# Kernel optimization log

Measured on AMD Instinct MI355X. Metric: run time of the kernel, lower is better.

Reference implementation:

```python
import jax, jax.numpy as jnp
import numpy as np

B, C, H, W = 16, 256, 96, 96
P = 16          # num_prototypes
G = 8           # GroupNorm groups
EPS = 1e-5


def setup_inputs() -> dict:
    key = jax.random.key(0)
    ks = jax.random.split(key, 18)
    n = jax.random.normal
    return {
        "x": n(ks[0], (B, C, H, W), jnp.float32),
        "prototypes": n(ks[1], (1, P, C), jnp.float32),
        "pos_embed": n(ks[2], (1, C, 64, 64), jnp.float32) * 0.02,
        "q_w": n(ks[3], (C, C), jnp.float32) * (C ** -0.5),
        "q_b": n(ks[4], (C,), jnp.float32) * 0.01,
        "k_w": n(ks[5], (C, C), jnp.float32) * (C ** -0.5),
        "k_b": n(ks[6], (C,), jnp.float32) * 0.01,
        "v_w": n(ks[7], (C, C), jnp.float32) * (C ** -0.5),
        "v_b": n(ks[8], (C,), jnp.float32) * 0.01,
        "out_w": n(ks[9], (C, C), jnp.float32) * (C ** -0.5),
        "out_b": n(ks[10], (C,), jnp.float32) * 0.01,
        "dw_w": n(ks[11], (C, 1, 3, 3), jnp.float32) * (1.0 / 3.0),  # depthwise 3x3, no bias
        "bn_g": 1.0 + 0.1 * n(ks[12], (C,), jnp.float32),
        "bn_b": 0.1 * n(ks[13], (C,), jnp.float32),
        "bn_mean": 0.05 * n(ks[14], (C,), jnp.float32),
        "bn_var": 0.5 + jax.random.uniform(ks[15], (C,), jnp.float32),
        "gn_g": 1.0 + 0.1 * n(ks[16], (C,), jnp.float32),
        "gn_b": 0.1 * n(ks[17], (C,), jnp.float32),
    }


def _forward(x, prototypes, pos_embed, q_w, q_b, k_w, k_b, v_w, v_b,
             out_w, out_b, dw_w, bn_g, bn_b, bn_mean, bn_var, gn_g, gn_b):
    b, c, h, w = x.shape
    residual = x

    # bilinear interpolation of learnable PE (half-pixel centers == align_corners=False)
    pos = jax.image.resize(pos_embed, (1, c, h, w), method="bilinear")
    xp = x + pos

    # 1x1 conv Q projection -> [B, HW, C]
    q = jnp.einsum("bchw,dc->bhwd", xp, q_w) + q_b          # [B,H,W,C]
    q = q.reshape(b, h * w, c)

    # K/V from tiny prototype set (shared across batch) -> [P, C]
    k = prototypes[0] @ k_w.T + k_b
    v = prototypes[0] @ v_w.T + v_b

    # attention over only P=16 keys
    scale = c ** (-0.5)
    attn = jax.nn.softmax(jnp.einsum("bnc,pc->bnp", q, k) * scale, axis=-1)
    out = jnp.einsum("bnp,pc->bnc", attn, v)                # [B,HW,C]
    out = out.reshape(b, h, w, c).transpose(0, 3, 1, 2)     # [B,C,H,W]

    # 1x1 conv out projection
    out = jnp.einsum("bchw,dc->bdhw", out, out_w) + out_b[None, :, None, None]

    # local branch: depthwise 3x3 conv -> BN (eval, running stats) -> GELU(exact)
    dw = jax.lax.conv_general_dilated(
        out, dw_w, window_strides=(1, 1), padding="SAME",
        feature_group_count=c, dimension_numbers=("NCHW", "OIHW", "NCHW"))
    inv = (bn_g / jnp.sqrt(bn_var + EPS))[None, :, None, None]
    bn = (dw - bn_mean[None, :, None, None]) * inv + bn_b[None, :, None, None]
    out = out + jax.nn.gelu(bn, approximate=False)

    # GroupNorm(8, C) over residual sum
    y = out + residual
    yg = y.reshape(b, G, c // G, h, w)
    mu = yg.mean(axis=(2, 3, 4), keepdims=True)
    var = yg.var(axis=(2, 3, 4), keepdims=True)
    yn = ((yg - mu) * jax.lax.rsqrt(var + EPS)).reshape(b, c, h, w)
    return yn * gn_g[None, :, None, None] + gn_b[None, :, None, None]


def reference(x, prototypes, pos_embed, q_w, q_b, k_w, k_b, v_w, v_b,
              out_w, out_b, dw_w, bn_g, bn_b, bn_mean, bn_var, gn_g, gn_b):
    return _forward(x, prototypes, pos_embed, q_w, q_b, k_w, k_b, v_w, v_b,
                    out_w, out_b, dw_w, bn_g, bn_b, bn_mean, bn_var, gn_g, gn_b)
```

## Files before the change

kernel.cpp:

```cpp
#include <hip/hip_runtime.h>
#include <math.h>

#define C_   256
#define B_   16
#define HW_  9216
#define W_   96
#define H_   96
#define P_   16
#define EPS_ 1e-5f

typedef unsigned int u32;

__device__ __forceinline__ float gelu_f(float v)
{
    const float z = fabsf(v) * 0.70710678118654752f;
    const float t = 1.0f / fmaf(0.3275911f, z, 1.0f);
    float poly = fmaf(1.061405429f, t, -1.453152027f);
    poly = fmaf(poly, t, 1.421413741f);
    poly = fmaf(poly, t, -0.284496736f);
    poly = fmaf(poly, t, 0.254829592f);
    poly *= t;
    const float e = __expf(-z * z);
    const float er = copysignf(1.0f - poly * e, v);
    return 0.5f * v * (1.0f + er);
}

__global__ __launch_bounds__(256) void k_kv(
    const float* __restrict__ proto, const float* __restrict__ kw,
    const float* __restrict__ kb, const float* __restrict__ vw,
    const float* __restrict__ vb, float* __restrict__ wk, float* __restrict__ wv,
    float* __restrict__ sums)
{
    __shared__ float pr[C_];
    const int p = blockIdx.x, d = threadIdx.x;
    if (p == 0) sums[d] = 0.f;
    pr[d] = proto[p * C_ + d];
    __syncthreads();
    float kk = kb[d], vv = vb[d];
    const float* kr = kw + d * C_;
    const float* vr = vw + d * C_;
    #pragma unroll 8
    for (int c = 0; c < C_; ++c) {
        const float pc = pr[c];
        kk = fmaf(pc, kr[c], kk);
        vv = fmaf(pc, vr[c], vv);
    }
    wk[p * C_ + d] = kk;
    wv[p * C_ + d] = vv;
}

__global__ __launch_bounds__(256) void k_mu(
    const float* __restrict__ wk, const float* __restrict__ wv,
    const float* __restrict__ qw, const float* __restrict__ qb,
    const float* __restrict__ ow,
    float* __restrict__ wm, float* __restrict__ wu, float* __restrict__ ws0)
{
    __shared__ float row[C_];
    __shared__ float red[C_];
    const int blk = blockIdx.x, t = threadIdx.x;
    if (blk < 16) {
        const int p = blk;
        row[t] = wk[p * C_ + t];
        __syncthreads();
        float mm = 0.f;
        #pragma unroll 8
        for (int d = 0; d < C_; ++d)
            mm = fmaf(row[d], qw[d * C_ + t], mm);
        wm[t * P_ + p] = mm;
        red[t] = qb[t] * row[t];
        __syncthreads();
        for (int s = 128; s > 0; s >>= 1) {
            if (t < s) red[t] += red[t + s];
            __syncthreads();
        }
        if (t == 0) ws0[p] = red[0];
    } else {
        const int p = blk - 16;
        row[t] = wv[p * C_ + t];
        __syncthreads();
        float uu = 0.f;
        const float* orow = ow + t * C_;
        #pragma unroll 8
        for (int c = 0; c < C_; ++c)
            uu = fmaf(row[c], orow[c], uu);
        wu[t * P_ + p] = uu;
    }
}

__global__ __launch_bounds__(256) void k_pd(
    const float* __restrict__ pos, const float* __restrict__ m,
    float* __restrict__ pd)
{
    const int n = blockIdx.x * 256 + threadIdx.x;
    const int h = n / W_, w = n - h * W_;
    float sy = (h + 0.5f) * (2.0f / 3.0f) - 0.5f;
    float sx = (w + 0.5f) * (2.0f / 3.0f) - 0.5f;
    sy = fminf(fmaxf(sy, 0.f), 63.f);
    sx = fminf(fmaxf(sx, 0.f), 63.f);
    const int y0 = (int)sy, x0 = (int)sx;
    const float fy = sy - (float)y0, fx = sx - (float)x0;
    const int y1 = min(y0 + 1, 63), x1 = min(x0 + 1, 63);
    const float w00 = (1.f - fy) * (1.f - fx), w01 = (1.f - fy) * fx;
    const float w10 = fy * (1.f - fx),         w11 = fy * fx;
    const int i00 = y0 * 64 + x0, i01 = y0 * 64 + x1;
    const int i10 = y1 * 64 + x0, i11 = y1 * 64 + x1;

    float acc[P_];
    #pragma unroll
    for (int p = 0; p < P_; ++p) acc[p] = 0.f;

    #pragma unroll 4
    for (int c = 0; c < C_; ++c) {
        const float* pc = pos + c * 4096;
        const float pv = pc[i00] * w00 + pc[i01] * w01 +
                         pc[i10] * w10 + pc[i11] * w11;
        #pragma unroll
        for (int p = 0; p < P_; ++p)
            acc[p] = fmaf(pv, m[c * P_ + p], acc[p]);
    }
    #pragma unroll
    for (int p = 0; p < P_; ++p) pd[p * HW_ + n] = acc[p];
}

__global__ __launch_bounds__(64) void k_logits(
    const float* __restrict__ x, const float* __restrict__ m,
    const float* __restrict__ s0, const float* __restrict__ pd,
    float* __restrict__ lw)
{
    const int n = blockIdx.x * 64 + threadIdx.x;
    const int b = n / HW_;
    const int npx = n - b * HW_;
    const float* xp = x + (size_t)b * (C_ * HW_) + npx;

    float acc[P_];
    #pragma unroll
    for (int p = 0; p < P_; ++p) acc[p] = 0.f;

    for (int cc = 0; cc < C_; cc += 16) {
        float xv[16];
        #pragma unroll
        for (int j = 0; j < 16; ++j)
            xv[j] = xp[(size_t)(cc + j) * HW_];
        #pragma unroll
        for (int j = 0; j < 16; ++j) {
            const float* mr = m + (cc + j) * P_;
            #pragma unroll
            for (int p = 0; p < P_; ++p)
                acc[p] = fmaf(xv[j], mr[p], acc[p]);
        }
    }

    float l[P_];
    float mx = -1e30f;
    #pragma unroll
    for (int p = 0; p < P_; ++p) {
        l[p] = (acc[p] + pd[(size_t)p * HW_ + npx] + s0[p]) * 0.0625f;
        mx = fmaxf(mx, l[p]);
    }
    float sum = 0.f;
    #pragma unroll
    for (int p = 0; p < P_; ++p) { l[p] = __expf(l[p] - mx); sum += l[p]; }
    const float r = 1.f / sum;

    float* lp = lw + (size_t)b * (P_ * HW_) + npx;
    #pragma unroll
    for (int p = 0; p < P_; ++p) lp[(size_t)p * HW_] = l[p] * r;
}

__global__ __launch_bounds__(256) void k_out(
    const float* __restrict__ lw, const float* __restrict__ u,
    const float* __restrict__ ob, float* __restrict__ o2)
{
    const int b = blockIdx.z;
    const int d0 = blockIdx.y * 16;
    const int px = blockIdx.x * 1024 + threadIdx.x * 4;

    const float* lp = lw + (size_t)b * (P_ * HW_) + px;
    float4 lv[P_];
    #pragma unroll
    for (int p = 0; p < P_; ++p)
        lv[p] = *reinterpret_cast<const float4*>(lp + (size_t)p * HW_);

    float* op = o2 + ((size_t)b * C_ + d0) * HW_ + px;
    #pragma unroll
    for (int j = 0; j < 16; ++j) {
        const int d = d0 + j;
        const float* ur = u + d * P_;
        const float obd = ob[d];
        float4 o = make_float4(obd, obd, obd, obd);
        #pragma unroll
        for (int p = 0; p < P_; ++p) {
            o.x = fmaf(lv[p].x, ur[p], o.x);
            o.y = fmaf(lv[p].y, ur[p], o.y);
            o.z = fmaf(lv[p].z, ur[p], o.z);
            o.w = fmaf(lv[p].w, ur[p], o.w);
        }
        *reinterpret_cast<float4*>(op + (size_t)j * HW_) = o;
    }
}

__global__ __launch_bounds__(256) void k_local(
    const float* __restrict__ x,
    const float* __restrict__ dww, const float* __restrict__ bng,
    const float* __restrict__ bnb, const float* __restrict__ bnm,
    const float* __restrict__ bnv,
    float* __restrict__ y, float* __restrict__ sums)
{
    __shared__ float tile[98 * 100];
    const int c = blockIdx.x, b = blockIdx.y, t = threadIdx.x;

    if (t < 100) { tile[t] = 0.f; tile[97 * 100 + t] = 0.f; }
    if (t < 96)  { tile[(t + 1) * 100 + 1] = 0.f; tile[(t + 1) * 100 + 98] = 0.f; }

    const size_t plane = (size_t)(b * C_ + c) * HW_;
    const float4* op4 = reinterpret_cast<const float4*>(y + plane);
    #pragma unroll
    for (int k = 0; k < 9; ++k) {
        const int g = t + k * 256;
        const int h = g / 24;
        const int w0 = (g - h * 24) * 4;
        const float4 v = op4[g];
        const int base = (h + 1) * 100 + w0 + 2;
        *reinterpret_cast<float2*>(&tile[base])     = make_float2(v.x, v.y);
        *reinterpret_cast<float2*>(&tile[base + 2]) = make_float2(v.z, v.w);
    }
    __syncthreads();

    const float w00 = dww[c * 9 + 0], w01 = dww[c * 9 + 1], w02 = dww[c * 9 + 2];
    const float w10 = dww[c * 9 + 3], w11 = dww[c * 9 + 4], w12 = dww[c * 9 + 5];
    const float w20 = dww[c * 9 + 6], w21 = dww[c * 9 + 7], w22 = dww[c * 9 + 8];
    const float inv  = bng[c] * rsqrtf(bnv[c] + EPS_);
    const float mu   = bnm[c];
    const float beta = bnb[c];

    const float4* xp4 = reinterpret_cast<const float4*>(x + plane);
    float4* yp4 = reinterpret_cast<float4*>(y + plane);
    float s1 = 0.f, s2 = 0.f;

    #pragma unroll
    for (int k = 0; k < 9; ++k) {
        const int g = t + k * 256;
        const float4 xv = xp4[g];
        const int h = g / 24;
        const int w0 = (g - h * 24) * 4;
        const int r0 = h * 100 + w0;
        const float4 a0 = *reinterpret_cast<const float4*>(&tile[r0]);
        const float4 a1 = *reinterpret_cast<const float4*>(&tile[r0 + 4]);
        const float4 b0 = *reinterpret_cast<const float4*>(&tile[r0 + 100]);
        const float4 b1 = *reinterpret_cast<const float4*>(&tile[r0 + 104]);
        const float4 c0 = *reinterpret_cast<const float4*>(&tile[r0 + 200]);
        const float4 c1 = *reinterpret_cast<const float4*>(&tile[r0 + 204]);
        const float A[8]  = {a0.x, a0.y, a0.z, a0.w, a1.x, a1.y, a1.z, a1.w};
        const float Bv[8] = {b0.x, b0.y, b0.z, b0.w, b1.x, b1.y, b1.z, b1.w};
        const float Cv[8] = {c0.x, c0.y, c0.z, c0.w, c1.x, c1.y, c1.z, c1.w};
        const float xs[4] = {xv.x, xv.y, xv.z, xv.w};
        float ys[4];
        #pragma unroll
        for (int j = 0; j < 4; ++j) {
            float dwv = A[j + 1] * w00 + A[j + 2] * w01 + A[j + 3] * w02
                      + Bv[j + 1] * w10 + Bv[j + 2] * w11 + Bv[j + 3] * w12
                      + Cv[j + 1] * w20 + Cv[j + 2] * w21 + Cv[j + 3] * w22;
            const float bn = (dwv - mu) * inv + beta;
            const float yv = Bv[j + 2] + gelu_f(bn) + xs[j];
            s1 += yv;
            s2 = fmaf(yv, yv, s2);
            ys[j] = yv;
        }
        yp4[g] = make_float4(ys[0], ys[1], ys[2], ys[3]);
    }

    __syncthreads();
    float* red = tile;
    red[t] = s1; red[256 + t] = s2;
    __syncthreads();
    for (int s = 128; s > 0; s >>= 1) {
        if (t < s) { red[t] += red[t + s]; red[256 + t] += red[256 + t + s]; }
        __syncthreads();
    }
    if (t == 0) {
        const int bg = b * 8 + (c >> 5);
        atomicAdd(&sums[bg * 2 + 0], red[0]);
        atomicAdd(&sums[bg * 2 + 1], red[256]);
    }
}

__global__ __launch_bounds__(256) void k_norm(
    const float* __restrict__ sums, const float* __restrict__ gng,
    const float* __restrict__ gnb, float* __restrict__ y)
{
    const u32 i0 = ((u32)blockIdx.x * 256u + threadIdx.x) * 4u;
    const u32 plane = i0 / HW_;
    const u32 c = plane & 255u;
    const u32 b = plane >> 8;
    const u32 bg = b * 8u + (c >> 5);
    const float cntinv = 1.f / 294912.f;
    const float mean = sums[bg * 2 + 0] * cntinv;
    const float var  = fmaf(sums[bg * 2 + 1], cntinv, -mean * mean);
    const float inv  = rsqrtf(var + EPS_);
    const float a  = gng[c] * inv;
    const float bb = gnb[c] - mean * a;

    float4 v = *reinterpret_cast<const float4*>(y + i0);
    v.x = fmaf(v.x, a, bb);
    v.y = fmaf(v.y, a, bb);
    v.z = fmaf(v.z, a, bb);
    v.w = fmaf(v.w, a, bb);
    *reinterpret_cast<float4*>(y + i0) = v;
}

extern "C" void kernel_launch(void* const* d_in, const int* in_sizes, int n_in,
                              void* d_out, int out_size, void* d_ws, size_t ws_size,
                              hipStream_t stream)
{
    const float* x     = (const float*)d_in[0];
    const float* proto = (const float*)d_in[1];
    const float* pos   = (const float*)d_in[2];
    const float* qw    = (const float*)d_in[3];
    const float* qb    = (const float*)d_in[4];
    const float* kw    = (const float*)d_in[5];
    const float* kb    = (const float*)d_in[6];
    const float* vw    = (const float*)d_in[7];
    const float* vb    = (const float*)d_in[8];
    const float* ow    = (const float*)d_in[9];
    const float* ob    = (const float*)d_in[10];
    const float* dww   = (const float*)d_in[11];
    const float* bng   = (const float*)d_in[12];
    const float* bnb   = (const float*)d_in[13];
    const float* bnm   = (const float*)d_in[14];
    const float* bnv   = (const float*)d_in[15];
    const float* gng   = (const float*)d_in[16];
    const float* gnb   = (const float*)d_in[17];

    char* ws = (char*)d_ws;
    float* sums = (float*)(ws);
    float* s0   = (float*)(ws + 1024);
    float* wk   = (float*)(ws + 2048);
    float* wv   = (float*)(ws + 2048 + 16384);
    float* wm   = (float*)(ws + 2048 + 2 * 16384);
    float* wu   = (float*)(ws + 2048 + 3 * 16384);
    float* pd   = (float*)(ws + 2048 + 4 * 16384);
    float* lw   = (float*)(ws + 2048 + 4 * 16384 + 589824);

    float* out = (float*)d_out;

    k_kv<<<16, 256, 0, stream>>>(proto, kw, kb, vw, vb, wk, wv, sums);
    k_mu<<<32, 256, 0, stream>>>(wk, wv, qw, qb, ow, wm, wu, s0);
    k_pd<<<36, 256, 0, stream>>>(pos, wm, pd);
    k_logits<<<2304, 64, 0, stream>>>(x, wm, s0, pd, lw);
    k_out<<<dim3(9, 16, 16), 256, 0, stream>>>(lw, wu, ob, out);
    k_local<<<dim3(256, 16), 256, 0, stream>>>(x, dww, bng, bnb, bnm, bnv, out, sums);
    k_norm<<<36864, 256, 0, stream>>>(sums, gng, gnb, out);
}
```

Baseline: 524.8 us.

## Fuse attention-output projection into depthwise local kernel; widen GroupNorm apply per thread

The out-projection (attention weights times U plus bias) is now computed directly into the shared-memory tile of the depthwise-conv kernel, one block per (channel, batch). This removes the separate k_out launch and the write and re-read of the full pre-conv output tensor. In exchange, each block re-reads all 16 attention-weight planes for its batch, so the small lw buffer is read 256 times (it should mostly hit cache). The GroupNorm apply kernel now has each thread process 16 floats instead of 4, with a quarter as many blocks.

```diff
diff --git a/kernel.cpp b/kernel.cpp
--- a/kernel.cpp
+++ b/kernel.cpp
@@ -167,40 +167,9 @@
     for (int p = 0; p < P_; ++p) lp[(size_t)p * HW_] = l[p] * r;
 }
 
-__global__ __launch_bounds__(256) void k_out(
+__global__ __launch_bounds__(256) void k_attnlocal(
     const float* __restrict__ lw, const float* __restrict__ u,
-    const float* __restrict__ ob, float* __restrict__ o2)
-{
-    const int b = blockIdx.z;
-    const int d0 = blockIdx.y * 16;
-    const int px = blockIdx.x * 1024 + threadIdx.x * 4;
-
-    const float* lp = lw + (size_t)b * (P_ * HW_) + px;
-    float4 lv[P_];
-    #pragma unroll
-    for (int p = 0; p < P_; ++p)
-        lv[p] = *reinterpret_cast<const float4*>(lp + (size_t)p * HW_);
-
-    float* op = o2 + ((size_t)b * C_ + d0) * HW_ + px;
-    #pragma unroll
-    for (int j = 0; j < 16; ++j) {
-        const int d = d0 + j;
-        const float* ur = u + d * P_;
-        const float obd = ob[d];
-        float4 o = make_float4(obd, obd, obd, obd);
-        #pragma unroll
-        for (int p = 0; p < P_; ++p) {
-            o.x = fmaf(lv[p].x, ur[p], o.x);
-            o.y = fmaf(lv[p].y, ur[p], o.y);
-            o.z = fmaf(lv[p].z, ur[p], o.z);
-            o.w = fmaf(lv[p].w, ur[p], o.w);
-        }
-        *reinterpret_cast<float4*>(op + (size_t)j * HW_) = o;
-    }
-}
-
-__global__ __launch_bounds__(256) void k_local(
-    const float* __restrict__ x,
+    const float* __restrict__ ob, const float* __restrict__ x,
     const float* __restrict__ dww, const float* __restrict__ bng,
     const float* __restrict__ bnb, const float* __restrict__ bnm,
     const float* __restrict__ bnv,
@@ -212,17 +181,32 @@
     if (t < 100) { tile[t] = 0.f; tile[97 * 100 + t] = 0.f; }
     if (t < 96)  { tile[(t + 1) * 100 + 1] = 0.f; tile[(t + 1) * 100 + 98] = 0.f; }
 
-    const size_t plane = (size_t)(b * C_ + c) * HW_;
-    const float4* op4 = reinterpret_cast<const float4*>(y + plane);
+    float uc[P_];
+    #pragma unroll
+    for (int p = 0; p < P_; ++p) uc[p] = u[c * P_ + p];
+    const float obc = ob[c];
+
+    const float* lp = lw + (size_t)b * (P_ * HW_);
     #pragma unroll
     for (int k = 0; k < 9; ++k) {
         const int g = t + k * 256;
+        float4 lv[P_];
+        #pragma unroll
+        for (int p = 0; p < P_; ++p)
+            lv[p] = *reinterpret_cast<const float4*>(lp + (size_t)p * HW_ + g * 4);
+        float4 o = make_float4(obc, obc, obc, obc);
+        #pragma unroll
+        for (int p = 0; p < P_; ++p) {
+            o.x = fmaf(lv[p].x, uc[p], o.x);
+            o.y = fmaf(lv[p].y, uc[p], o.y);
+            o.z = fmaf(lv[p].z, uc[p], o.z);
+            o.w = fmaf(lv[p].w, uc[p], o.w);
+        }
         const int h = g / 24;
         const int w0 = (g - h * 24) * 4;
-        const float4 v = op4[g];
         const int base = (h + 1) * 100 + w0 + 2;
-        *reinterpret_cast<float2*>(&tile[base])     = make_float2(v.x, v.y);
-        *reinterpret_cast<float2*>(&tile[base + 2]) = make_float2(v.z, v.w);
+        *reinterpret_cast<float2*>(&tile[base])     = make_float2(o.x, o.y);
+        *reinterpret_cast<float2*>(&tile[base + 2]) = make_float2(o.z, o.w);
     }
     __syncthreads();
 
@@ -233,6 +217,7 @@
     const float mu   = bnm[c];
     const float beta = bnb[c];
 
+    const size_t plane = (size_t)(b * C_ + c) * HW_;
     const float4* xp4 = reinterpret_cast<const float4*>(x + plane);
     float4* yp4 = reinterpret_cast<float4*>(y + plane);
     float s1 = 0.f, s2 = 0.f;
@@ -288,7 +273,7 @@
     const float* __restrict__ sums, const float* __restrict__ gng,
     const float* __restrict__ gnb, float* __restrict__ y)
 {
-    const u32 i0 = ((u32)blockIdx.x * 256u + threadIdx.x) * 4u;
+    const u32 i0 = ((u32)blockIdx.x * 256u + threadIdx.x) * 16u;
     const u32 plane = i0 / HW_;
     const u32 c = plane & 255u;
     const u32 b = plane >> 8;
@@ -300,12 +285,22 @@
     const float a  = gng[c] * inv;
     const float bb = gnb[c] - mean * a;
 
-    float4 v = *reinterpret_cast<const float4*>(y + i0);
-    v.x = fmaf(v.x, a, bb);
-    v.y = fmaf(v.y, a, bb);
-    v.z = fmaf(v.z, a, bb);
-    v.w = fmaf(v.w, a, bb);
-    *reinterpret_cast<float4*>(y + i0) = v;
+    float4 v0 = *reinterpret_cast<const float4*>(y + i0);
+    float4 v1 = *reinterpret_cast<const float4*>(y + i0 + 4);
+    float4 v2 = *reinterpret_cast<const float4*>(y + i0 + 8);
+    float4 v3 = *reinterpret_cast<const float4*>(y + i0 + 12);
+    v0.x = fmaf(v0.x, a, bb); v0.y = fmaf(v0.y, a, bb);
+    v0.z = fmaf(v0.z, a, bb); v0.w = fmaf(v0.w, a, bb);
+    v1.x = fmaf(v1.x, a, bb); v1.y = fmaf(v1.y, a, bb);
+    v1.z = fmaf(v1.z, a, bb); v1.w = fmaf(v1.w, a, bb);
+    v2.x = fmaf(v2.x, a, bb); v2.y = fmaf(v2.y, a, bb);
+    v2.z = fmaf(v2.z, a, bb); v2.w = fmaf(v2.w, a, bb);
+    v3.x = fmaf(v3.x, a, bb); v3.y = fmaf(v3.y, a, bb);
+    v3.z = fmaf(v3.z, a, bb); v3.w = fmaf(v3.w, a, bb);
+    *reinterpret_cast<float4*>(y + i0)      = v0;
+    *reinterpret_cast<float4*>(y + i0 + 4)  = v1;
+    *reinterpret_cast<float4*>(y + i0 + 8)  = v2;
+    *reinterpret_cast<float4*>(y + i0 + 12) = v3;
 }
 
 extern "C" void kernel_launch(void* const* d_in, const int* in_sizes, int n_in,
@@ -347,7 +342,7 @@
     k_mu<<<32, 256, 0, stream>>>(wk, wv, qw, qb, ow, wm, wu, s0);
     k_pd<<<36, 256, 0, stream>>>(pos, wm, pd);
     k_logits<<<2304, 64, 0, stream>>>(x, wm, s0, pd, lw);
-    k_out<<<dim3(9, 16, 16), 256, 0, stream>>>(lw, wu, ob, out);
-    k_local<<<dim3(256, 16), 256, 0, stream>>>(x, dww, bng, bnb, bnm, bnv, out, sums);
-    k_norm<<<36864, 256, 0, stream>>>(sums, gng, gnb, out);
-}
+    k_attnlocal<<<dim3(256, 16), 256, 0, stream>>>(lw, wu, ob, x, dww, bng, bnb,
+                                                   bnm, bnv, out, sums);
+    k_norm<<<9216, 256, 0, stream>>>(sums, gng, gnb, out);
+}
```

Result: slower. 556.6 us (+6.1%).
